# Optimization experiments

Measured on AMD Instinct MI355X. Metric: run time of the kernel, lower is better.

Reference implementation:

```python
import jax, jax.numpy as jnp
import numpy as np
from jax import lax

EPS = 1e-12  # F.normalize default eps
NUM_HEADS = 3
TEMP = 1.0

def setup_inputs() -> dict:
    key = jax.random.key(0)
    ks = jax.random.split(key, 7)
    b, c, h, w = 4, 96, 256, 256
    s = 0.02
    return {
        'x': jax.random.normal(ks[0], (b, c, h, w), jnp.float32),
        'qkv_w': jax.random.normal(ks[1], (3 * c, c), jnp.float32) * s,
        'qkv_b': jax.random.normal(ks[2], (3 * c,), jnp.float32) * s,
        'dw_w': jax.random.normal(ks[3], (3 * c, 1, 3, 3), jnp.float32) * s,
        'dw_b': jax.random.normal(ks[4], (3 * c,), jnp.float32) * s,
        'proj_w': jax.random.normal(ks[5], (c, c), jnp.float32) * s,
        'proj_b': jax.random.normal(ks[6], (c,), jnp.float32) * s,
    }

def _l2norm(t):
    # F.normalize over last dim: t / max(||t||, eps)
    n = jnp.sqrt(jnp.sum(t * t, axis=-1, keepdims=True))
    return t / jnp.maximum(n, EPS)

def reference(x, qkv_w, qkv_b, dw_w, dw_b, proj_w, proj_b):
    b, c, h, w = x.shape
    head = NUM_HEADS
    # 1x1 conv (pointwise) -> [b, 3c, h, w]
    qkv = jnp.einsum('oc,bchw->bohw', qkv_w, x) + qkv_b[None, :, None, None]
    # 3x3 depthwise conv, padding=1
    qkv = lax.conv_general_dilated(
        qkv, dw_w, window_strides=(1, 1), padding='SAME',
        feature_group_count=3 * c,
        dimension_numbers=('NCHW', 'OIHW', 'NCHW')) + dw_b[None, :, None, None]
    q, k, v = jnp.split(qkv, 3, axis=1)
    # b (head hc) h w -> b head hc (h w)
    def to_heads(t):
        return t.reshape(b, head, c // head, h * w)
    q, k, v = to_heads(q), to_heads(k), to_heads(v)
    q = _l2norm(q)
    k = _l2norm(k)
    # channel-wise attention scores: [b, head, hc, hc]
    attn = jnp.einsum('bhcn,bhdn->bhcd', q, k) * TEMP
    attn = jax.nn.softmax(attn, axis=-1)
    out = jnp.einsum('bhcd,bhdn->bhcn', attn, v)  # [b, head, hc, hw]
    out = out.reshape(b, c, h, w)
    out = jnp.einsum('oc,bchw->bohw', proj_w, out) + proj_b[None, :, None, None]
    return (out, attn)
```

## Files before the change

### kernel.cpp

```cpp
#include <hip/hip_runtime.h>
#include <hip/hip_bf16.h>

#define B_  4
#define C_  96
#define H_  256
#define W_  256
#define N_  (H_*W_)
#define C3_ 288
#define HEAD_ 3
#define HC_ 32
#define EPS_ 1e-12f
#define XP_ 104
#define SPLITS_ 128

typedef __attribute__((ext_vector_type(8))) short short8;
typedef __attribute__((ext_vector_type(4))) float f32x4;

__device__ __forceinline__ unsigned short f2bf(float f) {
  unsigned u = __float_as_uint(f);
  u += 0x7fffu + ((u >> 16) & 1u);
  return (unsigned short)(u >> 16);
}
__device__ __forceinline__ float bf2f(unsigned short h) {
  return __uint_as_float((unsigned)h << 16);
}
__device__ __forceinline__ float bf_lo(unsigned u) { return __uint_as_float(u << 16); }
__device__ __forceinline__ float bf_hi(unsigned u) { return __uint_as_float(u & 0xffff0000u); }
__device__ __forceinline__ unsigned pack_bf(float a, float b) {
  return (unsigned)f2bf(a) | ((unsigned)f2bf(b) << 16);
}

__global__ __launch_bounds__(256) void k_cast(
    const float* __restrict__ s, unsigned short* __restrict__ d, int n) {
  const int i = blockIdx.x * 256 + threadIdx.x;
  if (i < n) d[i] = f2bf(s[i]);
}

__global__ __launch_bounds__(256) void k1_mfma(
    const float* __restrict__ x, const unsigned short* __restrict__ wbf,
    const float* __restrict__ bias, unsigned short* __restrict__ out) {
  __shared__ unsigned short Wl[C3_ * XP_];
  __shared__ unsigned short Xt[32 * XP_];
  __shared__ float Bl[C3_];
  const int tid = threadIdx.x;
  const int b = blockIdx.y;
  for (int i = tid; i < C3_ * C_; i += 256) {
    const int c = i / 96, k = i % 96;
    Wl[c * XP_ + k] = wbf[i];
  }
  for (int i = tid; i < C3_; i += 256) Bl[i] = bias[i];
  const int lane = tid & 63;
  const int wv = tid >> 6;
  const int n0 = (wv & 1) * 16;
  const int mbase = (wv >> 1) * 144;
  const int l15 = lane & 15, quad = lane >> 4;
  for (int ti = blockIdx.x; ti < N_ / 32; ti += gridDim.x) {
    const int gp0 = ti * 32;
    __syncthreads();
    const float* xb = x + ((size_t)b * C_) * N_ + gp0;
#pragma unroll
    for (int l = 0; l < 12; ++l) {
      const int idx = tid + l * 256;
      const int c = idx >> 5, p = idx & 31;
      Xt[p * XP_ + c] = f2bf(xb[(size_t)c * N_ + p]);
    }
    __syncthreads();
    f32x4 acc[9];
#pragma unroll
    for (int m = 0; m < 9; ++m) acc[m] = (f32x4){0.f, 0.f, 0.f, 0.f};
#pragma unroll
    for (int kc = 0; kc < 3; ++kc) {
      const short8 bfr = *reinterpret_cast<const short8*>(&Xt[(n0 + l15) * XP_ + kc * 32 + quad * 8]);
#pragma unroll
      for (int m = 0; m < 9; ++m) {
        const short8 afr = *reinterpret_cast<const short8*>(
            &Wl[(mbase + m * 16 + l15) * XP_ + kc * 32 + quad * 8]);
        acc[m] = __builtin_amdgcn_mfma_f32_16x16x32_bf16(afr, bfr, acc[m], 0, 0, 0);
      }
    }
    unsigned short* ob = out + (size_t)b * C3_ * N_ + gp0 + n0 + l15;
#pragma unroll
    for (int m = 0; m < 9; ++m) {
      const int chb = mbase + m * 16 + quad * 4;
#pragma unroll
      for (int r = 0; r < 4; ++r)
        ob[(size_t)(chb + r) * N_] = f2bf(acc[m][r] + Bl[chb + r]);
    }
  }
}

__global__ __launch_bounds__(256) void k_dw_reg(
    unsigned short* a, const float* __restrict__ w9,
    const float* __restrict__ bias, float* __restrict__ inv) {
  const int bc = blockIdx.x;
  const int ch = bc % C3_;
  unsigned short* p = a + (size_t)bc * N_;
  const int tid = threadIdx.x;
  const int tr = tid >> 5;
  const int tc = tid & 31;
  const int x0 = tc * 8;
  const int y0 = tr * 32;
  float wv[9];
#pragma unroll
  for (int i = 0; i < 9; ++i) wv[i] = w9[ch * 9 + i];
  const float bv = bias[ch];

  auto load_row = [&](int y, float* d) {
    if ((unsigned)y >= 256u) {
#pragma unroll
      for (int j = 0; j < 10; ++j) d[j] = 0.f;
      return;
    }
    const unsigned short* rp = p + (size_t)y * W_;
    const uint4 u = *reinterpret_cast<const uint4*>(rp + x0);
    d[1] = bf_lo(u.x); d[2] = bf_hi(u.x); d[3] = bf_lo(u.y); d[4] = bf_hi(u.y);
    d[5] = bf_lo(u.z); d[6] = bf_hi(u.z); d[7] = bf_lo(u.w); d[8] = bf_hi(u.w);
    d[0] = (tc > 0) ? bf2f(rp[x0 - 1]) : 0.f;
    d[9] = (tc < 31) ? bf2f(rp[x0 + 8]) : 0.f;
  };

  float rm[10], rc[10], rn[10], rb[10];
  load_row(y0 - 1, rm);
  load_row(y0, rc);
  load_row(y0 + 1, rn);
  load_row(y0 + 32, rb);
  __syncthreads();

  float ss = 0.f;
  for (int y = y0; y < y0 + 32; ++y) {
    float o[8];
#pragma unroll
    for (int j = 0; j < 8; ++j) {
      o[j] = bv + wv[0] * rm[j] + wv[1] * rm[j + 1] + wv[2] * rm[j + 2]
                + wv[3] * rc[j] + wv[4] * rc[j + 1] + wv[5] * rc[j + 2]
                + wv[6] * rn[j] + wv[7] * rn[j + 1] + wv[8] * rn[j + 2];
      ss += o[j] * o[j];
    }
    uint4 st;
    st.x = pack_bf(o[0], o[1]); st.y = pack_bf(o[2], o[3]);
    st.z = pack_bf(o[4], o[5]); st.w = pack_bf(o[6], o[7]);
    *reinterpret_cast<uint4*>(p + (size_t)y * W_ + x0) = st;
#pragma unroll
    for (int j = 0; j < 10; ++j) { rm[j] = rc[j]; rc[j] = rn[j]; }
    const int ny = y + 2;
    if (ny <= y0 + 31) {
      load_row(ny, rn);
    } else if (ny == y0 + 32) {
#pragma unroll
      for (int j = 0; j < 10; ++j) rn[j] = rb[j];
    }
  }
#pragma unroll
  for (int off = 32; off > 0; off >>= 1) ss += __shfl_down(ss, off, 64);
  __shared__ float red[4];
  if ((tid & 63) == 0) red[tid >> 6] = ss;
  __syncthreads();
  if (tid == 0 && ch < 192) {
    const float t = red[0] + red[1] + red[2] + red[3];
    const int b = bc / C3_;
    inv[b * 192 + ch] = 1.0f / fmaxf(sqrtf(t), EPS_);
  }
}

__global__ __launch_bounds__(256) void k_attn_mfma(
    const unsigned short* __restrict__ dw, float* __restrict__ part) {
  const int tid = threadIdx.x;
  const int lane = tid & 63;
  const int wv = tid >> 6;
  const int i0 = (wv >> 1) * 16, j0 = (wv & 1) * 16;
  const int h = blockIdx.y, b = blockIdx.z;
  const int n0 = blockIdx.x * (N_ / SPLITS_);
  const int l15 = lane & 15, quad = lane >> 4;
  const unsigned short* qrow =
      dw + ((size_t)(b * C3_ + h * HC_ + i0 + l15)) * N_ + n0 + quad * 8;
  const unsigned short* krow =
      dw + ((size_t)(b * C3_ + C_ + h * HC_ + j0 + l15)) * N_ + n0 + quad * 8;
  f32x4 acc = (f32x4){0.f, 0.f, 0.f, 0.f};
#pragma unroll 4
  for (int s = 0; s < N_ / SPLITS_; s += 32) {
    const short8 af = *reinterpret_cast<const short8*>(qrow + s);
    const short8 bf = *reinterpret_cast<const short8*>(krow + s);
    acc = __builtin_amdgcn_mfma_f32_16x16x32_bf16(af, bf, acc, 0, 0, 0);
  }
  float* pp = part + (size_t)blockIdx.x * (B_ * HEAD_ * 1024)
                   + ((size_t)(b * HEAD_ + h)) * 1024;
#pragma unroll
  for (int r = 0; r < 4; ++r)
    pp[(i0 + quad * 4 + r) * 32 + j0 + l15] = acc[r];
}

__global__ __launch_bounds__(256) void k_softmax(
    const float* __restrict__ part, const float* __restrict__ inv,
    float* __restrict__ attn_out) {
  const int tid = threadIdx.x;
  const int R = blockIdx.x * 8 + (tid >> 5);
  const int j = tid & 31;
  const int b = R / 96, rem = R % 96;
  const int h = rem / 32, i = rem % 32;
  float v = 0.f;
  for (int s = 0; s < SPLITS_; ++s)
    v += part[(size_t)s * (B_ * HEAD_ * 1024) + R * 32 + j];
  const float invq = inv[b * 192 + h * 32 + i];
  const float invk = inv[b * 192 + 96 + h * 32 + j];
  v *= invq * invk;
  float m = v;
#pragma unroll
  for (int off = 16; off > 0; off >>= 1) m = fmaxf(m, __shfl_xor(m, off, 32));
  const float e = __expf(v - m);
  float s = e;
#pragma unroll
  for (int off = 16; off > 0; off >>= 1) s += __shfl_xor(s, off, 32);
  attn_out[R * 32 + j] = e / s;
}

__global__ __launch_bounds__(256) void k_attn_v(
    const unsigned short* __restrict__ dwv, const float* __restrict__ attn,
    unsigned short* __restrict__ out_mid) {
  __shared__ float as_[1024];
  const int tid = threadIdx.x;
  const int h = blockIdx.y, b = blockIdx.z;
  const int n = (blockIdx.x * 256 + tid) * 2;
  const float* ap = attn + ((size_t)(b * HEAD_ + h)) * 1024;
  for (int l = tid; l < 1024; l += 256) as_[l] = ap[l];
  __syncthreads();
  const unsigned short* vp = dwv + ((size_t)(b * C3_ + 2 * C_ + h * HC_)) * N_ + n;
  float a0[32], a1[32];
#pragma unroll
  for (int i = 0; i < 32; ++i) { a0[i] = 0.f; a1[i] = 0.f; }
#pragma unroll
  for (int j = 0; j < 32; ++j) {
    const unsigned u = *reinterpret_cast<const unsigned*>(vp + (size_t)j * N_);
    const float v0 = bf_lo(u), v1 = bf_hi(u);
#pragma unroll
    for (int i = 0; i < 32; ++i) {
      const float w = as_[i * 32 + j];
      a0[i] += w * v0; a1[i] += w * v1;
    }
  }
  unsigned short* op = out_mid + ((size_t)(b * C3_) + h * HC_) * N_ + n;
#pragma unroll
  for (int i = 0; i < 32; ++i)
    *reinterpret_cast<unsigned*>(op + (size_t)i * N_) = pack_bf(a0[i], a1[i]);
}

__global__ __launch_bounds__(256) void k7_mfma(
    const unsigned short* __restrict__ mid,
    const unsigned short* __restrict__ wbf,
    const float* __restrict__ bias, float* __restrict__ out) {
  __shared__ unsigned short Wl[C_ * XP_];
  __shared__ unsigned short Xt[64 * XP_];
  __shared__ float Bl[C_];
  const int tid = threadIdx.x;
  const int b = blockIdx.y;
  for (int i = tid; i < C_ * C_; i += 256) {
    const int c = i / 96, k = i % 96;
    Wl[c * XP_ + k] = wbf[i];
  }
  if (tid < C_) Bl[tid] = bias[tid];
  const int lane = tid & 63;
  const int wv = tid >> 6;
  const int n0 = wv * 16;
  const int l15 = lane & 15, quad = lane >> 4;
  for (int ti = blockIdx.x; ti < N_ / 64; ti += gridDim.x) {
    const int gp0 = ti * 64;
    __syncthreads();
    const unsigned short* xb = mid + (size_t)b * C3_ * N_ + gp0;
#pragma unroll
    for (int l = 0; l < 24; ++l) {
      const int idx = tid + l * 256;
      const int c = idx >> 6, p = idx & 63;
      Xt[p * XP_ + c] = xb[(size_t)c * N_ + p];
    }
    __syncthreads();
    f32x4 acc[6];
#pragma unroll
    for (int m = 0; m < 6; ++m) acc[m] = (f32x4){0.f, 0.f, 0.f, 0.f};
#pragma unroll
    for (int kc = 0; kc < 3; ++kc) {
      const short8 bfr = *reinterpret_cast<const short8*>(&Xt[(n0 + l15) * XP_ + kc * 32 + quad * 8]);
#pragma unroll
      for (int m = 0; m < 6; ++m) {
        const short8 afr = *reinterpret_cast<const short8*>(
            &Wl[(m * 16 + l15) * XP_ + kc * 32 + quad * 8]);
        acc[m] = __builtin_amdgcn_mfma_f32_16x16x32_bf16(afr, bfr, acc[m], 0, 0, 0);
      }
    }
    float* ob = out + (size_t)b * C_ * N_ + gp0 + n0 + l15;
#pragma unroll
    for (int m = 0; m < 6; ++m) {
      const int chb = m * 16 + quad * 4;
#pragma unroll
      for (int r = 0; r < 4; ++r)
        ob[(size_t)(chb + r) * N_] = acc[m][r] + Bl[chb + r];
    }
  }
}

extern "C" void kernel_launch(void* const* d_in, const int* in_sizes, int n_in,
                              void* d_out, int out_size, void* d_ws, size_t ws_size,
                              hipStream_t stream) {
  const float* x      = (const float*)d_in[0];
  const float* qkv_w  = (const float*)d_in[1];
  const float* qkv_b  = (const float*)d_in[2];
  const float* dw_w   = (const float*)d_in[3];
  const float* dw_b   = (const float*)d_in[4];
  const float* proj_w = (const float*)d_in[5];
  const float* proj_b = (const float*)d_in[6];

  float* out      = (float*)d_out;
  float* attn_out = out + (size_t)B_ * C_ * N_;

  unsigned short* A = (unsigned short*)d_ws;
  float* inv   = (float*)(A + (size_t)B_ * C3_ * N_);
  float* part  = inv + 768;
  unsigned short* wq_bf = (unsigned short*)(part + SPLITS_ * B_ * HEAD_ * 1024);
  unsigned short* wp_bf = wq_bf + C3_ * C_;

  k_cast<<<108, 256, 0, stream>>>(qkv_w, wq_bf, C3_ * C_);
  k_cast<<<36, 256, 0, stream>>>(proj_w, wp_bf, C_ * C_);
  k1_mfma<<<dim3(512, B_), 256, 0, stream>>>(x, wq_bf, qkv_b, A);
  k_dw_reg<<<B_ * C3_, 256, 0, stream>>>(A, dw_w, dw_b, inv);
  k_attn_mfma<<<dim3(SPLITS_, HEAD_, B_), 256, 0, stream>>>(A, part);
  k_softmax<<<48, 256, 0, stream>>>(part, inv, attn_out);
  k_attn_v<<<dim3(N_ / 512, HEAD_, B_), 256, 0, stream>>>(A, attn_out, A);
  k7_mfma<<<dim3(256, B_), 256, 0, stream>>>(A, wp_bf, proj_b, out);
}
```

Before: 382.0 us.

## Fold attention-weighted V into projection via per-batch combined weight matrix

Precomputes M = proj_w · blockdiag(attn) per batch in a small kernel, so the final projection reads V directly and the separate attn·V pass and its intermediate buffer round trip are removed. Both 1x1-conv MFMA kernels are also rewritten to load the pixel-column fragments straight into registers and read the weights from global memory, dropping the LDS staging and the persistent grid loops. The cost is strided per-element global loads for the B fragments, and the attention matrix is now rounded to bf16 inside M.

```diff
diff --git a/kernel.cpp b/kernel.cpp
--- a/kernel.cpp
+++ b/kernel.cpp
@@ -10,7 +10,6 @@
 #define HEAD_ 3
 #define HC_ 32
 #define EPS_ 1e-12f
-#define XP_ 104
 #define SPLITS_ 128
 
 typedef __attribute__((ext_vector_type(8))) short short8;
@@ -39,53 +38,39 @@
 __global__ __launch_bounds__(256) void k1_mfma(
     const float* __restrict__ x, const unsigned short* __restrict__ wbf,
     const float* __restrict__ bias, unsigned short* __restrict__ out) {
-  __shared__ unsigned short Wl[C3_ * XP_];
-  __shared__ unsigned short Xt[32 * XP_];
-  __shared__ float Bl[C3_];
   const int tid = threadIdx.x;
   const int b = blockIdx.y;
-  for (int i = tid; i < C3_ * C_; i += 256) {
-    const int c = i / 96, k = i % 96;
-    Wl[c * XP_ + k] = wbf[i];
-  }
-  for (int i = tid; i < C3_; i += 256) Bl[i] = bias[i];
   const int lane = tid & 63;
   const int wv = tid >> 6;
-  const int n0 = (wv & 1) * 16;
-  const int mbase = (wv >> 1) * 144;
   const int l15 = lane & 15, quad = lane >> 4;
-  for (int ti = blockIdx.x; ti < N_ / 32; ti += gridDim.x) {
-    const int gp0 = ti * 32;
-    __syncthreads();
-    const float* xb = x + ((size_t)b * C_) * N_ + gp0;
-#pragma unroll
-    for (int l = 0; l < 12; ++l) {
-      const int idx = tid + l * 256;
-      const int c = idx >> 5, p = idx & 31;
-      Xt[p * XP_ + c] = f2bf(xb[(size_t)c * N_ + p]);
-    }
-    __syncthreads();
-    f32x4 acc[9];
-#pragma unroll
-    for (int m = 0; m < 9; ++m) acc[m] = (f32x4){0.f, 0.f, 0.f, 0.f};
+  const int gpix = blockIdx.x * 64 + wv * 16 + l15;
+  const float* xcol = x + (size_t)b * C_ * N_ + gpix;
+  short8 bfr[3];
+#pragma unroll
+  for (int kc = 0; kc < 3; ++kc) {
+#pragma unroll
+    for (int u = 0; u < 8; ++u)
+      bfr[kc][u] = (short)f2bf(xcol[(size_t)(kc * 32 + quad * 8 + u) * N_]);
+  }
+  f32x4 acc[18];
+#pragma unroll
+  for (int m = 0; m < 18; ++m) acc[m] = (f32x4){0.f, 0.f, 0.f, 0.f};
+#pragma unroll
+  for (int m = 0; m < 18; ++m) {
 #pragma unroll
     for (int kc = 0; kc < 3; ++kc) {
-      const short8 bfr = *reinterpret_cast<const short8*>(&Xt[(n0 + l15) * XP_ + kc * 32 + quad * 8]);
-#pragma unroll
-      for (int m = 0; m < 9; ++m) {
-        const short8 afr = *reinterpret_cast<const short8*>(
-            &Wl[(mbase + m * 16 + l15) * XP_ + kc * 32 + quad * 8]);
-        acc[m] = __builtin_amdgcn_mfma_f32_16x16x32_bf16(afr, bfr, acc[m], 0, 0, 0);
-      }
-    }
-    unsigned short* ob = out + (size_t)b * C3_ * N_ + gp0 + n0 + l15;
-#pragma unroll
-    for (int m = 0; m < 9; ++m) {
-      const int chb = mbase + m * 16 + quad * 4;
-#pragma unroll
-      for (int r = 0; r < 4; ++r)
-        ob[(size_t)(chb + r) * N_] = f2bf(acc[m][r] + Bl[chb + r]);
-    }
+      const short8 afr = *reinterpret_cast<const short8*>(
+          wbf + (m * 16 + l15) * C_ + kc * 32 + quad * 8);
+      acc[m] = __builtin_amdgcn_mfma_f32_16x16x32_bf16(afr, bfr[kc], acc[m], 0, 0, 0);
+    }
+  }
+  unsigned short* ob = out + (size_t)b * C3_ * N_ + gpix;
+#pragma unroll
+  for (int m = 0; m < 18; ++m) {
+    const int chb = m * 16 + quad * 4;
+#pragma unroll
+    for (int r = 0; r < 4; ++r)
+      ob[(size_t)(chb + r) * N_] = f2bf(acc[m][r] + bias[chb + r]);
   }
 }
 
@@ -213,86 +198,64 @@
   attn_out[R * 32 + j] = e / s;
 }
 
-__global__ __launch_bounds__(256) void k_attn_v(
-    const unsigned short* __restrict__ dwv, const float* __restrict__ attn,
-    unsigned short* __restrict__ out_mid) {
-  __shared__ float as_[1024];
-  const int tid = threadIdx.x;
-  const int h = blockIdx.y, b = blockIdx.z;
-  const int n = (blockIdx.x * 256 + tid) * 2;
-  const float* ap = attn + ((size_t)(b * HEAD_ + h)) * 1024;
-  for (int l = tid; l < 1024; l += 256) as_[l] = ap[l];
+__global__ __launch_bounds__(256) void k_M(
+    const float* __restrict__ attn, const float* __restrict__ proj_w,
+    unsigned short* __restrict__ Mbf) {
+  const int b = blockIdx.x;
+  const int tid = threadIdx.x;
+  __shared__ float As[HEAD_ * 1024];
+  for (int l = tid; l < HEAD_ * 1024; l += 256)
+    As[l] = attn[(size_t)b * HEAD_ * 1024 + l];
   __syncthreads();
-  const unsigned short* vp = dwv + ((size_t)(b * C3_ + 2 * C_ + h * HC_)) * N_ + n;
-  float a0[32], a1[32];
-#pragma unroll
-  for (int i = 0; i < 32; ++i) { a0[i] = 0.f; a1[i] = 0.f; }
-#pragma unroll
-  for (int j = 0; j < 32; ++j) {
-    const unsigned u = *reinterpret_cast<const unsigned*>(vp + (size_t)j * N_);
-    const float v0 = bf_lo(u), v1 = bf_hi(u);
-#pragma unroll
-    for (int i = 0; i < 32; ++i) {
-      const float w = as_[i * 32 + j];
-      a0[i] += w * v0; a1[i] += w * v1;
-    }
-  }
-  unsigned short* op = out_mid + ((size_t)(b * C3_) + h * HC_) * N_ + n;
-#pragma unroll
-  for (int i = 0; i < 32; ++i)
-    *reinterpret_cast<unsigned*>(op + (size_t)i * N_) = pack_bf(a0[i], a1[i]);
+  for (int e = tid; e < C_ * C_; e += 256) {
+    const int o = e / 96, jj = e % 96;
+    const int h = jj >> 5, j = jj & 31;
+    float s = 0.f;
+#pragma unroll
+    for (int i = 0; i < 32; ++i)
+      s += proj_w[o * 96 + h * 32 + i] * As[h * 1024 + i * 32 + j];
+    Mbf[(size_t)b * C_ * C_ + e] = f2bf(s);
+  }
 }
 
 __global__ __launch_bounds__(256) void k7_mfma(
-    const unsigned short* __restrict__ mid,
-    const unsigned short* __restrict__ wbf,
+    const unsigned short* __restrict__ A ,
+    const unsigned short* __restrict__ Mbf,
     const float* __restrict__ bias, float* __restrict__ out) {
-  __shared__ unsigned short Wl[C_ * XP_];
-  __shared__ unsigned short Xt[64 * XP_];
-  __shared__ float Bl[C_];
   const int tid = threadIdx.x;
   const int b = blockIdx.y;
-  for (int i = tid; i < C_ * C_; i += 256) {
-    const int c = i / 96, k = i % 96;
-    Wl[c * XP_ + k] = wbf[i];
-  }
-  if (tid < C_) Bl[tid] = bias[tid];
   const int lane = tid & 63;
   const int wv = tid >> 6;
-  const int n0 = wv * 16;
   const int l15 = lane & 15, quad = lane >> 4;
-  for (int ti = blockIdx.x; ti < N_ / 64; ti += gridDim.x) {
-    const int gp0 = ti * 64;
-    __syncthreads();
-    const unsigned short* xb = mid + (size_t)b * C3_ * N_ + gp0;
-#pragma unroll
-    for (int l = 0; l < 24; ++l) {
-      const int idx = tid + l * 256;
-      const int c = idx >> 6, p = idx & 63;
-      Xt[p * XP_ + c] = xb[(size_t)c * N_ + p];
-    }
-    __syncthreads();
-    f32x4 acc[6];
-#pragma unroll
-    for (int m = 0; m < 6; ++m) acc[m] = (f32x4){0.f, 0.f, 0.f, 0.f};
+  const int gpix = blockIdx.x * 64 + wv * 16 + l15;
+  const unsigned short* vcol = A + ((size_t)(b * C3_ + 2 * C_)) * N_ + gpix;
+  const unsigned short* Mb = Mbf + (size_t)b * C_ * C_;
+  short8 bfr[3];
+#pragma unroll
+  for (int kc = 0; kc < 3; ++kc) {
+#pragma unroll
+    for (int u = 0; u < 8; ++u)
+      bfr[kc][u] = (short)vcol[(size_t)(kc * 32 + quad * 8 + u) * N_];
+  }
+  f32x4 acc[6];
+#pragma unroll
+  for (int m = 0; m < 6; ++m) acc[m] = (f32x4){0.f, 0.f, 0.f, 0.f};
+#pragma unroll
+  for (int m = 0; m < 6; ++m) {
 #pragma unroll
     for (int kc = 0; kc < 3; ++kc) {
-      const short8 bfr = *reinterpret_cast<const short8*>(&Xt[(n0 + l15) * XP_ + kc * 32 + quad * 8]);
-#pragma unroll
-      for (int m = 0; m < 6; ++m) {
-        const short8 afr = *reinterpret_cast<const short8*>(
-            &Wl[(m * 16 + l15) * XP_ + kc * 32 + quad * 8]);
-        acc[m] = __builtin_amdgcn_mfma_f32_16x16x32_bf16(afr, bfr, acc[m], 0, 0, 0);
-      }
-    }
-    float* ob = out + (size_t)b * C_ * N_ + gp0 + n0 + l15;
-#pragma unroll
-    for (int m = 0; m < 6; ++m) {
-      const int chb = m * 16 + quad * 4;
-#pragma unroll
-      for (int r = 0; r < 4; ++r)
-        ob[(size_t)(chb + r) * N_] = acc[m][r] + Bl[chb + r];
-    }
+      const short8 afr = *reinterpret_cast<const short8*>(
+          Mb + (m * 16 + l15) * C_ + kc * 32 + quad * 8);
+      acc[m] = __builtin_amdgcn_mfma_f32_16x16x32_bf16(afr, bfr[kc], acc[m], 0, 0, 0);
+    }
+  }
+  float* ob = out + (size_t)b * C_ * N_ + gpix;
+#pragma unroll
+  for (int m = 0; m < 6; ++m) {
+    const int chb = m * 16 + quad * 4;
+#pragma unroll
+    for (int r = 0; r < 4; ++r)
+      ob[(size_t)(chb + r) * N_] = acc[m][r] + bias[chb + r];
   }
 }
 
@@ -314,14 +277,13 @@
   float* inv   = (float*)(A + (size_t)B_ * C3_ * N_);
   float* part  = inv + 768;
   unsigned short* wq_bf = (unsigned short*)(part + SPLITS_ * B_ * HEAD_ * 1024);
-  unsigned short* wp_bf = wq_bf + C3_ * C_;
+  unsigned short* Mbf   = wq_bf + C3_ * C_;
 
   k_cast<<<108, 256, 0, stream>>>(qkv_w, wq_bf, C3_ * C_);
-  k_cast<<<36, 256, 0, stream>>>(proj_w, wp_bf, C_ * C_);
-  k1_mfma<<<dim3(512, B_), 256, 0, stream>>>(x, wq_bf, qkv_b, A);
+  k1_mfma<<<dim3(N_ / 64, B_), 256, 0, stream>>>(x, wq_bf, qkv_b, A);
   k_dw_reg<<<B_ * C3_, 256, 0, stream>>>(A, dw_w, dw_b, inv);
   k_attn_mfma<<<dim3(SPLITS_, HEAD_, B_), 256, 0, stream>>>(A, part);
   k_softmax<<<48, 256, 0, stream>>>(part, inv, attn_out);
-  k_attn_v<<<dim3(N_ / 512, HEAD_, B_), 256, 0, stream>>>(A, attn_out, A);
-  k7_mfma<<<dim3(256, B_), 256, 0, stream>>>(A, wp_bf, proj_b, out);
-}
+  k_M<<<B_, 256, 0, stream>>>(attn_out, proj_w, Mbf);
+  k7_mfma<<<dim3(N_ / 64, B_), 256, 0, stream>>>(A, Mbf, proj_b, out);
+}
```

Result: slower. 411.4 us (+7.7%).
